# Optimization experiments

Hardware: AMD Instinct MI355X
Metric: run time of the kernel (lower is better)

## Reference

```python
import jax, jax.numpy as jnp
import numpy as np

EPS = 1e-5

def _bn_train(h, gamma, beta):
    # BatchNorm1d in training mode: batch mean and biased variance over batch dim
    mu = jnp.mean(h, axis=0)
    var = jnp.mean((h - mu) ** 2, axis=0)
    return (h - mu) * jax.lax.rsqrt(var + EPS) * gamma + beta

def setup_inputs() -> dict:
    key = jax.random.key(0)
    ks = jax.random.split(key, 12)
    B, IN, H1, H2, NC = 16384, 4096, 256, 128, 12
    x = jax.random.normal(ks[0], (B, 1, 64, 64), dtype=jnp.float32)
    y = jax.random.randint(ks[1], (B,), 0, NC, dtype=jnp.int32)
    s1 = 1.0 / np.sqrt(IN)
    W1 = jax.random.uniform(ks[2], (H1, IN), jnp.float32, -s1, s1)
    b1 = jax.random.uniform(ks[3], (H1,), jnp.float32, -s1, s1)
    g1 = jax.random.normal(ks[4], (H1,), jnp.float32) * 0.1 + 1.0
    be1 = jax.random.normal(ks[5], (H1,), jnp.float32) * 0.1
    s2 = 1.0 / np.sqrt(H1)
    W2 = jax.random.uniform(ks[6], (H2, H1), jnp.float32, -s2, s2)
    b2 = jax.random.uniform(ks[7], (H2,), jnp.float32, -s2, s2)
    g2 = jax.random.normal(ks[8], (H2,), jnp.float32) * 0.1 + 1.0
    be2 = jax.random.normal(ks[9], (H2,), jnp.float32) * 0.1
    s4 = 1.0 / np.sqrt(H2)
    W4 = jax.random.uniform(ks[10], (NC, H2), jnp.float32, -s4, s4)
    b4 = jax.random.uniform(ks[11], (NC,), jnp.float32, -s4, s4)
    return {"x": x, "W1": W1, "b1": b1, "g1": g1, "be1": be1,
            "W2": W2, "b2": b2, "g2": g2, "be2": be2,
            "W4": W4, "b4": b4, "y": y}

def reference(x, W1, b1, g1, be1, W2, b2, g2, be2, W4, b4, y):
    B = x.shape[0]
    h = x.reshape(B, -1)  # [B, 4096]
    # layer 1: binarized linear + BN(train) + hardtanh (dropout p=0 is identity)
    h = h @ jnp.sign(W1).T + jnp.sign(b1)
    h = jnp.clip(_bn_train(h, g1, be1), -1.0, 1.0)
    # layer 2
    h = h @ jnp.sign(W2).T + jnp.sign(b2)
    h = jnp.clip(_bn_train(h, g2, be2), -1.0, 1.0)
    # final float linear
    return h @ W4.T + b4  # [B, 12]
```

## Files before the change

### kernel.cpp

```cpp
#include <hip/hip_runtime.h>
#include <cstddef>

typedef __attribute__((ext_vector_type(8))) short short8;
typedef __attribute__((ext_vector_type(4))) float f4;
typedef __attribute__((ext_vector_type(4))) unsigned int u4;

__device__ __forceinline__ unsigned int f2bf(float f){
  unsigned int u = __float_as_uint(f);
  u += 0x7fffu + ((u >> 16) & 1u);
  return u >> 16;
}
__device__ __forceinline__ float bflo(unsigned int w){ return __uint_as_float((w & 0xFFFFu) << 16); }
__device__ __forceinline__ float bfhi(unsigned int w){ return __uint_as_float(w & 0xFFFF0000u); }
__device__ __forceinline__ float fsign(float x){ return (x > 0.f) ? 1.f : ((x < 0.f) ? -1.f : 0.f); }
__device__ __forceinline__ float hclip(float x){ return fminf(1.f, fmaxf(-1.f, x)); }

#define BARRIER() do { \
    __builtin_amdgcn_sched_barrier(0); \
    asm volatile("s_waitcnt lgkmcnt(0)" ::: "memory"); \
    __builtin_amdgcn_s_barrier(); \
    asm volatile("" ::: "memory"); \
    __builtin_amdgcn_sched_barrier(0); \
  } while(0)

#define VBAR(N) do { \
    __builtin_amdgcn_sched_barrier(0); \
    asm volatile("s_waitcnt vmcnt(" #N ") lgkmcnt(0)" ::: "memory"); \
    __builtin_amdgcn_s_barrier(); \
    asm volatile("" ::: "memory"); \
    __builtin_amdgcn_sched_barrier(0); \
  } while(0)

#define GL16(gp, lp) __builtin_amdgcn_global_load_lds( \
    (const __attribute__((address_space(1))) void*)(gp), \
    (__attribute__((address_space(3))) void*)(lp), 16, 0, 0)

__global__ void prep_sign_k(const float* __restrict__ W1, unsigned short* __restrict__ w1s,
                            const float* __restrict__ W2, unsigned short* __restrict__ w2s){
  int i = (blockIdx.x * blockDim.x + threadIdx.x) * 8;
  const float* w; unsigned short* o; int off;
  if (i < 1048576){ w = W1; o = w1s; off = i; }
  else            { w = W2; o = w2s; off = i - 1048576; if (off >= 32768) return; }
  f4 a = *(const f4*)(w + off);
  f4 b = *(const f4*)(w + off + 4);
  unsigned short s[8];
  #pragma unroll
  for (int j = 0; j < 4; j++) s[j]   = (a[j] > 0.f) ? 0x3F80u : ((a[j] < 0.f) ? 0xBF80u : 0u);
  #pragma unroll
  for (int j = 0; j < 4; j++) s[4+j] = (b[j] > 0.f) ? 0x3F80u : ((b[j] < 0.f) ? 0xBF80u : 0u);
  u4 v;
  v.x = (unsigned)s[0] | ((unsigned)s[1] << 16);
  v.y = (unsigned)s[2] | ((unsigned)s[3] << 16);
  v.z = (unsigned)s[4] | ((unsigned)s[5] << 16);
  v.w = (unsigned)s[6] | ((unsigned)s[7] << 16);
  *(u4*)(o + off) = v;
}

__global__ __launch_bounds__(512, 1) void gemm1_k(
    const float* __restrict__ x, const unsigned short* __restrict__ w1s,
    const float* __restrict__ b1, unsigned short* __restrict__ h1,
    float* __restrict__ part1s, float* __restrict__ part1q)
{
  __shared__ __align__(16) char lds[147456];
  const int tid  = threadIdx.x;
  const int lane = tid & 63;
  const int wid  = tid >> 6;
  const int wm   = wid >> 2;
  const int wn   = wid & 3;
  const int cl   = lane & 15;
  const int g    = lane >> 4;
  const int row0 = blockIdx.x * 64;

  const int am  = tid >> 3;
  const int ak0 = (tid & 7) * 8;
  const float* xA = x + (size_t)(row0 + am) * 4096 + ak0;
  const int aw = (am * 128 + ak0 * 2) ^ ((am & 7) << 4);

  const int boff_o = tid * 16;

  f4 acc[2][4];
  const f4 z = {0.f, 0.f, 0.f, 0.f};
  #pragma unroll
  for (int i = 0; i < 2; i++)
    #pragma unroll
    for (int j = 0; j < 4; j++) acc[i][j] = z;

  f4 rA0_0, rA0_1, rA1_0, rA1_1, rA2_0, rA2_1;

#define ISSUEA(S, KB) do { \
    rA##S##_0 = *(const f4*)(xA + (KB)*64); \
    rA##S##_1 = *(const f4*)(xA + (KB)*64 + 4); \
  } while(0)

#define ISSUEB(BSLOT, KB) do { \
    char* _dst = lds + 16384 + (BSLOT)*32768; \
    _Pragma("unroll") \
    for (int c = 0; c < 4; c++){ \
      int _o  = c*8192 + boff_o; \
      int _n  = _o >> 7; \
      int _kb = (_o & 127) ^ ((_n & 7) << 4); \
      GL16((const char*)w1s + (size_t)_n*8192 + (size_t)(KB)*128 + _kb, _dst + _o); \
    } } while(0)

#define PACKA(S, ABUF) do { \
    u4 _v; \
    _v.x = f2bf(rA##S##_0[0]) | (f2bf(rA##S##_0[1]) << 16); \
    _v.y = f2bf(rA##S##_0[2]) | (f2bf(rA##S##_0[3]) << 16); \
    _v.z = f2bf(rA##S##_1[0]) | (f2bf(rA##S##_1[1]) << 16); \
    _v.w = f2bf(rA##S##_1[2]) | (f2bf(rA##S##_1[3]) << 16); \
    *(u4*)(lds + (ABUF)*8192 + aw) = _v; \
  } while(0)

#define COMPUTE(ABASE, BBASE) do { \
    const char* _ab = (const char*)(ABASE); \
    const char* _bb = (const char*)(BBASE); \
    short8 _af[2][2]; short8 _bf[4][2]; \
    _Pragma("unroll") \
    for (int fm = 0; fm < 2; fm++){ \
      int _m = wm*32 + fm*16 + cl; \
      _Pragma("unroll") \
      for (int ks = 0; ks < 2; ks++) \
        _af[fm][ks] = *(const short8*)(_ab + ((_m*128 + ks*64 + g*16) ^ ((_m & 7) << 4))); \
    } \
    _Pragma("unroll") \
    for (int fn = 0; fn < 4; fn++){ \
      int _n = wn*64 + fn*16 + cl; \
      _Pragma("unroll") \
      for (int ks = 0; ks < 2; ks++) \
        _bf[fn][ks] = *(const short8*)(_bb + ((_n*128 + ks*64 + g*16) ^ ((_n & 7) << 4))); \
    } \
    _Pragma("unroll") \
    for (int ks = 0; ks < 2; ks++) \
      _Pragma("unroll") \
      for (int fm = 0; fm < 2; fm++) \
        _Pragma("unroll") \
        for (int fn = 0; fn < 4; fn++) \
          acc[fm][fn] = __builtin_amdgcn_mfma_f32_16x16x32_bf16(_af[fm][ks], _bf[fn][ks], acc[fm][fn], 0, 0, 0); \
  } while(0)

#define STEP(K, SI, SP) do { \
    const int _k3 = (K) + 3; \
    const int _kc = (_k3 > 63) ? 63 : _k3; \
    ISSUEA(SI, _kc); \
    ISSUEB(_k3 & 3, _kc); \
    __builtin_amdgcn_sched_barrier(0); \
    COMPUTE(lds + ((K) & 1) * 8192, lds + 16384 + ((K) & 3) * 32768); \
    __builtin_amdgcn_sched_barrier(0); \
    PACKA(SP, ((K) + 1) & 1); \
    VBAR(12); \
  } while(0)

  ISSUEA(0, 0); ISSUEB(0, 0);
  ISSUEA(1, 1); ISSUEB(1, 1);
  ISSUEA(2, 2); ISSUEB(2, 2);
  PACKA(0, 0);
  VBAR(12);

  for (int kk = 0; kk < 63; kk += 3){
    STEP(kk,     0, 1);
    STEP(kk + 1, 1, 2);
    STEP(kk + 2, 2, 0);
  }
  COMPUTE(lds + 8192, lds + 16384 + 3 * 32768);
  asm volatile("s_waitcnt vmcnt(0)" ::: "memory");

#undef STEP
#undef COMPUTE
#undef PACKA
#undef ISSUEB
#undef ISSUEA

  #pragma unroll
  for (int fn = 0; fn < 4; fn++){
    int c = wn * 64 + fn * 16 + cl;
    float sb = fsign(b1[c]);
    float s = 0.f, q = 0.f;
    #pragma unroll
    for (int fm = 0; fm < 2; fm++){
      int rbase = row0 + wm * 32 + fm * 16 + g * 4;
      #pragma unroll
      for (int i = 0; i < 4; i++){
        float v = acc[fm][fn][i] + sb;
        h1[(size_t)(rbase + i) * 256 + c] = (unsigned short)f2bf(v);
        s += v; q += v * v;
      }
    }
    s += __shfl_xor(s, 16, 64); s += __shfl_xor(s, 32, 64);
    q += __shfl_xor(q, 16, 64); q += __shfl_xor(q, 32, 64);
    if (g == 0){
      part1s[c * 512 + blockIdx.x * 2 + wm] = s;
      part1q[c * 512 + blockIdx.x * 2 + wm] = q;
    }
  }
}

template<int COLS, int NBLK>
__global__ __launch_bounds__(64) void params_k(
    const float* __restrict__ ps, const float* __restrict__ pq,
    const float* __restrict__ g, const float* __restrict__ be,
    float* __restrict__ ab){
  int j = blockIdx.x * 64 + threadIdx.x;
  const f4* vs = (const f4*)(ps + (size_t)j * NBLK);
  const f4* vq = (const f4*)(pq + (size_t)j * NBLK);
  f4 s4 = {0,0,0,0}, q4 = {0,0,0,0};
  #pragma unroll 8
  for (int b = 0; b < NBLK/4; b++){ s4 += vs[b]; q4 += vq[b]; }
  float s = s4[0]+s4[1]+s4[2]+s4[3];
  float q = q4[0]+q4[1]+q4[2]+q4[3];
  float mu  = s * (1.f/16384.f);
  float var = q * (1.f/16384.f) - mu*mu;
  float a   = g[j] * rsqrtf(var + 1e-5f);
  ab[j] = a;
  ab[COLS + j] = be[j] - mu*a;
}

__global__ __launch_bounds__(512) void gemm2_k(
    const unsigned short* __restrict__ h1, const unsigned short* __restrict__ w2s,
    const float* __restrict__ b2, const float* __restrict__ ab1,
    unsigned short* __restrict__ h2, float* __restrict__ part2s, float* __restrict__ part2q)
{
  __shared__ __align__(16) char lds[32768];
  __shared__ __align__(16) float a1l[256];
  __shared__ __align__(16) float c1l[256];
  const int tid  = threadIdx.x;
  const int lane = tid & 63;
  const int wid  = tid >> 6;
  const int cl   = lane & 15;
  const int g    = lane >> 4;
  const int klo  = g * 8;
  const int row0 = blockIdx.x * 64;

  if (tid < 256) a1l[tid] = ab1[tid];
  else           c1l[tid - 256] = ab1[tid];

  const int am  = tid >> 3;
  const int ak0 = (tid & 7) * 8;
  const unsigned short* hA = h1 + (size_t)(row0 + am) * 256 + ak0;
  const int aw = ((am * 128) + (ak0 * 2)) ^ ((am & 7) << 4);
  const unsigned short* wbase = w2s + (size_t)(wid * 16 + cl) * 256 + klo;

  u4 q0 = *(const u4*)(hA);
  u4 q1 = *(const u4*)(hA + 64);
  u4 q2 = *(const u4*)(hA + 128);
  u4 q3 = *(const u4*)(hA + 192);
  short8 Bq0, Bq1, Br0, Br1;
  Bq0 = *(const short8*)(wbase);
  Bq1 = *(const short8*)(wbase + 32);

  BARRIER();

#define TRW(KB, RAW) do { \
    f4 _a0 = *(const f4*)(&a1l[(KB)*64 + ak0]); \
    f4 _a1 = *(const f4*)(&a1l[(KB)*64 + ak0 + 4]); \
    f4 _c0 = *(const f4*)(&c1l[(KB)*64 + ak0]); \
    f4 _c1 = *(const f4*)(&c1l[(KB)*64 + ak0 + 4]); \
    float _t0 = hclip(_a0[0]*bflo(RAW.x) + _c0[0]); \
    float _t1 = hclip(_a0[1]*bfhi(RAW.x) + _c0[1]); \
    float _t2 = hclip(_a0[2]*bflo(RAW.y) + _c0[2]); \
    float _t3 = hclip(_a0[3]*bfhi(RAW.y) + _c0[3]); \
    float _t4 = hclip(_a1[0]*bflo(RAW.z) + _c1[0]); \
    float _t5 = hclip(_a1[1]*bfhi(RAW.z) + _c1[1]); \
    float _t6 = hclip(_a1[2]*bflo(RAW.w) + _c1[2]); \
    float _t7 = hclip(_a1[3]*bfhi(RAW.w) + _c1[3]); \
    u4 _v; \
    _v.x = f2bf(_t0) | (f2bf(_t1) << 16); \
    _v.y = f2bf(_t2) | (f2bf(_t3) << 16); \
    _v.z = f2bf(_t4) | (f2bf(_t5) << 16); \
    _v.w = f2bf(_t6) | (f2bf(_t7) << 16); \
    *(u4*)(lds + (KB)*8192 + aw) = _v; \
  } while(0)

  TRW(0, q0); TRW(1, q1); TRW(2, q2); TRW(3, q3);
#undef TRW
  BARRIER();

  f4 acc[4];
  const f4 z = {0.f, 0.f, 0.f, 0.f};
  #pragma unroll
  for (int i = 0; i < 4; i++) acc[i] = z;

#define LOADB2(P, KB) do { \
    B##P##0 = *(const short8*)(wbase + (KB)*64); \
    B##P##1 = *(const short8*)(wbase + (KB)*64 + 32); \
  } while(0)

#define COMP2(BASE, P) do { \
    const char* _ab = (const char*)(BASE); \
    short8 _af[4][2]; \
    _Pragma("unroll") \
    for (int fm = 0; fm < 4; fm++){ \
      int _m = fm*16 + cl; \
      _af[fm][0] = *(const short8*)(_ab + ((_m*128 + klo*2) ^ ((_m & 7) << 4))); \
      _af[fm][1] = *(const short8*)(_ab + ((_m*128 + (32 + klo)*2) ^ ((_m & 7) << 4))); \
    } \
    _Pragma("unroll") \
    for (int fm = 0; fm < 4; fm++){ \
      acc[fm] = __builtin_amdgcn_mfma_f32_16x16x32_bf16(_af[fm][0], B##P##0, acc[fm], 0, 0, 0); \
      acc[fm] = __builtin_amdgcn_mfma_f32_16x16x32_bf16(_af[fm][1], B##P##1, acc[fm], 0, 0, 0); \
    } \
  } while(0)

  LOADB2(r, 1);
  COMP2(lds,         q);
  LOADB2(q, 2);
  COMP2(lds +  8192, r);
  LOADB2(r, 3);
  COMP2(lds + 16384, q);
  COMP2(lds + 24576, r);
#undef COMP2
#undef LOADB2

  {
    int c = wid*16 + cl;
    float sb = fsign(b2[c]);
    float s = 0.f, q = 0.f;
    #pragma unroll
    for (int fm = 0; fm < 4; fm++){
      int rbase = row0 + fm*16 + g*4;
      #pragma unroll
      for (int i = 0; i < 4; i++){
        float v = acc[fm][i] + sb;
        h2[(size_t)(rbase + i)*128 + c] = (unsigned short)f2bf(v);
        s += v; q += v*v;
      }
    }
    s += __shfl_xor(s, 16, 64); s += __shfl_xor(s, 32, 64);
    q += __shfl_xor(q, 16, 64); q += __shfl_xor(q, 32, 64);
    if (g == 0){
      part2s[c*256 + blockIdx.x] = s;
      part2q[c*256 + blockIdx.x] = q;
    }
  }
}

__global__ __launch_bounds__(128) void final_k(
    const unsigned short* __restrict__ h2,
    const float* __restrict__ part2s, const float* __restrict__ part2q,
    const float* __restrict__ g2, const float* __restrict__ be2,
    const float* __restrict__ W4, const float* __restrict__ b4,
    float* __restrict__ out)
{
  __shared__ __align__(16) float W4l[12*128];
  __shared__ __align__(16) float a2l[128];
  __shared__ __align__(16) float c2l[128];
  const int t = threadIdx.x;
  #pragma unroll
  for (int i = 0; i < 3; i++)
    *(f4*)&W4l[(i*128 + t)*4] = *(const f4*)(W4 + (i*128 + t)*4);
  {
    const f4* vs = (const f4*)(part2s + t*256);
    const f4* vq = (const f4*)(part2q + t*256);
    f4 s4 = {0,0,0,0}, q4 = {0,0,0,0};
    #pragma unroll 8
    for (int b = 0; b < 64; b++){ s4 += vs[b]; q4 += vq[b]; }
    float s = s4[0]+s4[1]+s4[2]+s4[3];
    float q = q4[0]+q4[1]+q4[2]+q4[3];
    float mu  = s * (1.f/16384.f);
    float var = q * (1.f/16384.f) - mu*mu;
    float a   = g2[t] * rsqrtf(var + 1e-5f);
    a2l[t] = a;
    c2l[t] = be2[t] - mu*a;
  }
  __syncthreads();

  const int r = blockIdx.x * 128 + t;
  const u4* hp = (const u4*)(h2 + (size_t)r * 128);
  u4 hv0 = hp[0], hv1 = hp[1], hv2 = hp[2],  hv3 = hp[3];
  u4 hv4 = hp[4], hv5 = hp[5], hv6 = hp[6],  hv7 = hp[7];
  u4 hv8 = hp[8], hv9 = hp[9], hv10 = hp[10], hv11 = hp[11];
  u4 hv12 = hp[12], hv13 = hp[13], hv14 = hp[14], hv15 = hp[15];

  float acc[12];
  #pragma unroll
  for (int o = 0; o < 12; o++) acc[o] = b4[o];

#define FPROC(HV, J) do { \
    f4 a0 = *(const f4*)&a2l[(J)*8];     f4 a1 = *(const f4*)&a2l[(J)*8 + 4]; \
    f4 c0 = *(const f4*)&c2l[(J)*8];     f4 c1 = *(const f4*)&c2l[(J)*8 + 4]; \
    float tt0 = hclip(a0[0]*bflo(HV.x) + c0[0]); \
    float tt1 = hclip(a0[1]*bfhi(HV.x) + c0[1]); \
    float tt2 = hclip(a0[2]*bflo(HV.y) + c0[2]); \
    float tt3 = hclip(a0[3]*bfhi(HV.y) + c0[3]); \
    float tt4 = hclip(a1[0]*bflo(HV.z) + c1[0]); \
    float tt5 = hclip(a1[1]*bfhi(HV.z) + c1[1]); \
    float tt6 = hclip(a1[2]*bflo(HV.w) + c1[2]); \
    float tt7 = hclip(a1[3]*bfhi(HV.w) + c1[3]); \
    _Pragma("unroll") \
    for (int o = 0; o < 12; o++){ \
      f4 w0 = *(const f4*)&W4l[o*128 + (J)*8]; \
      f4 w1 = *(const f4*)&W4l[o*128 + (J)*8 + 4]; \
      acc[o] += tt0*w0[0] + tt1*w0[1] + tt2*w0[2] + tt3*w0[3] \
              + tt4*w1[0] + tt5*w1[1] + tt6*w1[2] + tt7*w1[3]; \
    } \
  } while(0)

  FPROC(hv0, 0);  FPROC(hv1, 1);  FPROC(hv2, 2);   FPROC(hv3, 3);
  FPROC(hv4, 4);  FPROC(hv5, 5);  FPROC(hv6, 6);   FPROC(hv7, 7);
  FPROC(hv8, 8);  FPROC(hv9, 9);  FPROC(hv10, 10); FPROC(hv11, 11);
  FPROC(hv12, 12); FPROC(hv13, 13); FPROC(hv14, 14); FPROC(hv15, 15);
#undef FPROC

  #pragma unroll
  for (int o = 0; o < 12; o++) out[(size_t)r*12 + o] = acc[o];
}

extern "C" void kernel_launch(void* const* d_in, const int* in_sizes, int n_in,
                              void* d_out, int out_size, void* d_ws, size_t ws_size,
                              hipStream_t stream)
{
  const float* x   = (const float*)d_in[0];
  const float* W1  = (const float*)d_in[1];
  const float* b1  = (const float*)d_in[2];
  const float* g1  = (const float*)d_in[3];
  const float* be1 = (const float*)d_in[4];
  const float* W2  = (const float*)d_in[5];
  const float* b2  = (const float*)d_in[6];
  const float* g2  = (const float*)d_in[7];
  const float* be2 = (const float*)d_in[8];
  const float* W4  = (const float*)d_in[9];
  const float* b4  = (const float*)d_in[10];
  float* out = (float*)d_out;

  char* ws = (char*)d_ws;
  unsigned short* h1     = (unsigned short*)(ws);
  unsigned short* h2     = (unsigned short*)(ws + 8388608);
  unsigned short* w1s    = (unsigned short*)(ws + 12582912);
  unsigned short* w2s    = (unsigned short*)(ws + 14680064);
  float*          part1s = (float*)(ws + 14745600);
  float*          part1q = (float*)(ws + 15269888);
  float*          part2s = (float*)(ws + 15794176);
  float*          part2q = (float*)(ws + 15925248);
  float*          ab1    = (float*)(ws + 16056320);

  prep_sign_k<<<528, 256, 0, stream>>>(W1, w1s, W2, w2s);
  gemm1_k<<<256, 512, 0, stream>>>(x, w1s, b1, h1, part1s, part1q);
  params_k<256, 512><<<4, 64, 0, stream>>>(part1s, part1q, g1, be1, ab1);
  gemm2_k<<<256, 512, 0, stream>>>(h1, w2s, b2, ab1, h2, part2s, part2q);
  final_k<<<128, 128, 0, stream>>>(h2, part2s, part2q, g2, be2, W4, b4, out);
}
```

Baseline: 121.1 us.

## Shrink gemm1 row tile to 32 with double buffering for multi-block occupancy

gemm1 now processes 32 rows per block instead of 64, launches 512 blocks, and drops from a 4-stage to a 2-stage LDS pipeline. LDS use is halved so launch bounds allow several blocks per CU. Each wave now owns 32 output columns across all 32 rows. The goal is more concurrent blocks and better latency hiding across blocks, but the W1 sign tile is now re-streamed from global/L2 twice as often and per-block prefetch depth is shallower.

```diff
diff --git a/kernel.cpp b/kernel.cpp
--- a/kernel.cpp
+++ b/kernel.cpp
@@ -4,6 +4,7 @@
 typedef __attribute__((ext_vector_type(8))) short short8;
 typedef __attribute__((ext_vector_type(4))) float f4;
 typedef __attribute__((ext_vector_type(4))) unsigned int u4;
+typedef __attribute__((ext_vector_type(2))) unsigned int u2;
 
 __device__ __forceinline__ unsigned int f2bf(float f){
   unsigned int u = __float_as_uint(f);
@@ -15,20 +16,22 @@
 __device__ __forceinline__ float fsign(float x){ return (x > 0.f) ? 1.f : ((x < 0.f) ? -1.f : 0.f); }
 __device__ __forceinline__ float hclip(float x){ return fminf(1.f, fmaxf(-1.f, x)); }
 
+#define SB0 __builtin_amdgcn_sched_barrier(0)
+
 #define BARRIER() do { \
-    __builtin_amdgcn_sched_barrier(0); \
+    SB0; \
     asm volatile("s_waitcnt lgkmcnt(0)" ::: "memory"); \
     __builtin_amdgcn_s_barrier(); \
     asm volatile("" ::: "memory"); \
-    __builtin_amdgcn_sched_barrier(0); \
+    SB0; \
   } while(0)
 
 #define VBAR(N) do { \
-    __builtin_amdgcn_sched_barrier(0); \
+    SB0; \
     asm volatile("s_waitcnt vmcnt(" #N ") lgkmcnt(0)" ::: "memory"); \
     __builtin_amdgcn_s_barrier(); \
     asm volatile("" ::: "memory"); \
-    __builtin_amdgcn_sched_barrier(0); \
+    SB0; \
   } while(0)
 
 #define GL16(gp, lp) __builtin_amdgcn_global_load_lds( \
@@ -56,75 +59,64 @@
   *(u4*)(o + off) = v;
 }
 
-__global__ __launch_bounds__(512, 1) void gemm1_k(
+__global__ __launch_bounds__(512, 4) void gemm1_k(
     const float* __restrict__ x, const unsigned short* __restrict__ w1s,
     const float* __restrict__ b1, unsigned short* __restrict__ h1,
     float* __restrict__ part1s, float* __restrict__ part1q)
 {
-  __shared__ __align__(16) char lds[147456];
+  __shared__ __align__(16) char lds[73728];
   const int tid  = threadIdx.x;
   const int lane = tid & 63;
   const int wid  = tid >> 6;
-  const int wm   = wid >> 2;
-  const int wn   = wid & 3;
   const int cl   = lane & 15;
   const int g    = lane >> 4;
-  const int row0 = blockIdx.x * 64;
-
-  const int am  = tid >> 3;
-  const int ak0 = (tid & 7) * 8;
-  const float* xA = x + (size_t)(row0 + am) * 4096 + ak0;
-  const int aw = (am * 128 + ak0 * 2) ^ ((am & 7) << 4);
-
-  const int boff_o = tid * 16;
-
-  f4 acc[2][4];
+  const int row0 = blockIdx.x * 32;
+
+  const int am = tid >> 4;
+  const int kf = (tid & 15) * 4;
+  const float* xA = x + (size_t)(row0 + am) * 4096 + kf;
+  const int aw = (am * 128 + kf * 2) ^ ((am & 7) << 4);
+
+  f4 acc[2][2];
   const f4 z = {0.f, 0.f, 0.f, 0.f};
   #pragma unroll
-  for (int i = 0; i < 2; i++)
-    #pragma unroll
-    for (int j = 0; j < 4; j++) acc[i][j] = z;
-
-  f4 rA0_0, rA0_1, rA1_0, rA1_1, rA2_0, rA2_1;
-
-#define ISSUEA(S, KB) do { \
-    rA##S##_0 = *(const f4*)(xA + (KB)*64); \
-    rA##S##_1 = *(const f4*)(xA + (KB)*64 + 4); \
-  } while(0)
-
-#define ISSUEB(BSLOT, KB) do { \
-    char* _dst = lds + 16384 + (BSLOT)*32768; \
-    _Pragma("unroll") \
-    for (int c = 0; c < 4; c++){ \
-      int _o  = c*8192 + boff_o; \
+  for (int i = 0; i < 2; i++){ acc[i][0] = z; acc[i][1] = z; }
+
+  f4 rA0, rA1;
+
+#define ISSUEA(S, KB) do { rA##S = *(const f4*)(xA + (KB)*64); } while(0)
+
+#define ISSUEB(BUF, KB) do { \
+    char* _dst = lds + 8192 + (BUF)*32768; \
+    _Pragma("unroll") \
+    for (int _c = 0; _c < 4; _c++){ \
+      int _o  = _c*8192 + tid*16; \
       int _n  = _o >> 7; \
       int _kb = (_o & 127) ^ ((_n & 7) << 4); \
       GL16((const char*)w1s + (size_t)_n*8192 + (size_t)(KB)*128 + _kb, _dst + _o); \
     } } while(0)
 
 #define PACKA(S, ABUF) do { \
-    u4 _v; \
-    _v.x = f2bf(rA##S##_0[0]) | (f2bf(rA##S##_0[1]) << 16); \
-    _v.y = f2bf(rA##S##_0[2]) | (f2bf(rA##S##_0[3]) << 16); \
-    _v.z = f2bf(rA##S##_1[0]) | (f2bf(rA##S##_1[1]) << 16); \
-    _v.w = f2bf(rA##S##_1[2]) | (f2bf(rA##S##_1[3]) << 16); \
-    *(u4*)(lds + (ABUF)*8192 + aw) = _v; \
-  } while(0)
-
-#define COMPUTE(ABASE, BBASE) do { \
-    const char* _ab = (const char*)(ABASE); \
-    const char* _bb = (const char*)(BBASE); \
-    short8 _af[2][2]; short8 _bf[4][2]; \
+    u2 _v; \
+    _v.x = f2bf(rA##S[0]) | (f2bf(rA##S[1]) << 16); \
+    _v.y = f2bf(rA##S[2]) | (f2bf(rA##S[3]) << 16); \
+    *(u2*)(lds + (ABUF)*4096 + aw) = _v; \
+  } while(0)
+
+#define COMPUTE(BUF) do { \
+    const char* _ab = lds + (BUF)*4096; \
+    const char* _bb = lds + 8192 + (BUF)*32768; \
+    short8 _af[2][2]; short8 _bf[2][2]; \
     _Pragma("unroll") \
     for (int fm = 0; fm < 2; fm++){ \
-      int _m = wm*32 + fm*16 + cl; \
+      int _m = fm*16 + cl; \
       _Pragma("unroll") \
       for (int ks = 0; ks < 2; ks++) \
         _af[fm][ks] = *(const short8*)(_ab + ((_m*128 + ks*64 + g*16) ^ ((_m & 7) << 4))); \
     } \
     _Pragma("unroll") \
-    for (int fn = 0; fn < 4; fn++){ \
-      int _n = wn*64 + fn*16 + cl; \
+    for (int fn = 0; fn < 2; fn++){ \
+      int _n = wid*32 + fn*16 + cl; \
       _Pragma("unroll") \
       for (int ks = 0; ks < 2; ks++) \
         _bf[fn][ks] = *(const short8*)(_bb + ((_n*128 + ks*64 + g*16) ^ ((_n & 7) << 4))); \
@@ -134,50 +126,46 @@
       _Pragma("unroll") \
       for (int fm = 0; fm < 2; fm++) \
         _Pragma("unroll") \
-        for (int fn = 0; fn < 4; fn++) \
+        for (int fn = 0; fn < 2; fn++) \
           acc[fm][fn] = __builtin_amdgcn_mfma_f32_16x16x32_bf16(_af[fm][ks], _bf[fn][ks], acc[fm][fn], 0, 0, 0); \
   } while(0)
 
-#define STEP(K, SI, SP) do { \
-    const int _k3 = (K) + 3; \
-    const int _kc = (_k3 > 63) ? 63 : _k3; \
-    ISSUEA(SI, _kc); \
-    ISSUEB(_k3 & 3, _kc); \
-    __builtin_amdgcn_sched_barrier(0); \
-    COMPUTE(lds + ((K) & 1) * 8192, lds + 16384 + ((K) & 3) * 32768); \
-    __builtin_amdgcn_sched_barrier(0); \
-    PACKA(SP, ((K) + 1) & 1); \
-    VBAR(12); \
-  } while(0)
-
-  ISSUEA(0, 0); ISSUEB(0, 0);
-  ISSUEA(1, 1); ISSUEB(1, 1);
-  ISSUEA(2, 2); ISSUEB(2, 2);
+  ISSUEB(0, 0);
+  ISSUEA(0, 0);
+  ISSUEA(1, 1);
+  SB0;
   PACKA(0, 0);
-  VBAR(12);
-
-  for (int kk = 0; kk < 63; kk += 3){
-    STEP(kk,     0, 1);
-    STEP(kk + 1, 1, 2);
-    STEP(kk + 2, 2, 0);
+  VBAR(1);
+
+  for (int k = 0; k < 64; k += 2){
+    if (k < 63) ISSUEB(1, k + 1);
+    if (k < 62) ISSUEA(0, k + 2);
+    SB0;
+    COMPUTE(0);
+    SB0;
+    if (k < 63) PACKA(1, 1);
+    if (k < 62)      VBAR(1);
+    else if (k < 63) VBAR(0);
+    if (k + 1 < 63) ISSUEB(0, k + 2);
+    if (k + 1 < 62) ISSUEA(1, k + 3);
+    SB0;
+    COMPUTE(1);
+    SB0;
+    if (k + 1 < 63){ PACKA(0, 0); VBAR(1); }
   }
-  COMPUTE(lds + 8192, lds + 16384 + 3 * 32768);
-  asm volatile("s_waitcnt vmcnt(0)" ::: "memory");
-
-#undef STEP
 #undef COMPUTE
 #undef PACKA
 #undef ISSUEB
 #undef ISSUEA
 
   #pragma unroll
-  for (int fn = 0; fn < 4; fn++){
-    int c = wn * 64 + fn * 16 + cl;
+  for (int fn = 0; fn < 2; fn++){
+    int c = wid * 32 + fn * 16 + cl;
     float sb = fsign(b1[c]);
     float s = 0.f, q = 0.f;
     #pragma unroll
     for (int fm = 0; fm < 2; fm++){
-      int rbase = row0 + wm * 32 + fm * 16 + g * 4;
+      int rbase = row0 + fm * 16 + g * 4;
       #pragma unroll
       for (int i = 0; i < 4; i++){
         float v = acc[fm][fn][i] + sb;
@@ -188,8 +176,8 @@
     s += __shfl_xor(s, 16, 64); s += __shfl_xor(s, 32, 64);
     q += __shfl_xor(q, 16, 64); q += __shfl_xor(q, 32, 64);
     if (g == 0){
-      part1s[c * 512 + blockIdx.x * 2 + wm] = s;
-      part1q[c * 512 + blockIdx.x * 2 + wm] = q;
+      part1s[(size_t)c * 512 + blockIdx.x] = s;
+      part1q[(size_t)c * 512 + blockIdx.x] = q;
     }
   }
 }
@@ -433,7 +421,7 @@
   float*          ab1    = (float*)(ws + 16056320);
 
   prep_sign_k<<<528, 256, 0, stream>>>(W1, w1s, W2, w2s);
-  gemm1_k<<<256, 512, 0, stream>>>(x, w1s, b1, h1, part1s, part1q);
+  gemm1_k<<<512, 512, 0, stream>>>(x, w1s, b1, h1, part1s, part1q);
   params_k<256, 512><<<4, 64, 0, stream>>>(part1s, part1q, g1, be1, ab1);
   gemm2_k<<<256, 512, 0, stream>>>(h1, w2s, b2, ab1, h2, part2s, part2q);
   final_k<<<128, 128, 0, stream>>>(h2, part2s, part2q, g2, be2, W4, b4, out);
```

Result: slower. 132.8 us (+9.6%).
